# Performance work log

Hardware: AMD Instinct MI355X
Metric: run time of the kernel (lower is better)

## Reference

```python
import jax, jax.numpy as jnp
import numpy as np

B, Wd, C, H, F = 48, 88, 256, 32, 1024
NH_SELF, NH_CROSS = 8, 8


def _ln(x, g, b, eps=1e-5):
    mu = x.mean(-1, keepdims=True)
    var = ((x - mu) ** 2).mean(-1, keepdims=True)
    return (x - mu) / jnp.sqrt(var + eps) * g + b


def setup_inputs() -> dict:
    key = jax.random.key(0)
    ks = jax.random.split(key, 16)
    s = 0.02  # weight init scale
    d = {
        'pooled_features': jax.random.normal(ks[0], (B, Wd, C), jnp.float32),
        'features': jax.random.normal(ks[1], (B, C, H, Wd), jnp.float32),
        'self_pe': jax.random.normal(ks[2], (Wd, C), jnp.float32),
        'cross_pe': jax.random.normal(ks[3], (H, C), jnp.float32),
    }
    # LayerNorm params
    for n in ['ln_qs', 'ln_vs', 'ln_qc', 'ln_kv', 'ln_vc', 'ln_ffn']:
        d[n + '_g'] = jnp.ones((C,), jnp.float32)
        d[n + '_b'] = jnp.zeros((C,), jnp.float32)
    # attention projections (stored [in,out]; y = x @ W + b)
    names = ['Wq_s', 'Wk_s', 'Wv_s', 'Wp_s', 'Wq_c', 'Wk_c', 'Wv_c', 'Wp_c']
    for i, n in enumerate(names):
        d[n] = jax.random.normal(ks[4 + i], (C, C), jnp.float32) * s
    for n in ['bq_s', 'bv_s', 'bp_s', 'bq_c', 'bv_c', 'bp_c']:
        d[n] = jnp.zeros((C,), jnp.float32)
    # FFN
    d['W1'] = jax.random.normal(ks[12], (C, F), jnp.float32) * s
    d['b1'] = jnp.zeros((F,), jnp.float32)
    d['W2'] = jax.random.normal(ks[13], (F, C), jnp.float32) * s
    d['b2'] = jnp.zeros((C,), jnp.float32)
    return d


def reference(pooled_features, features, self_pe, cross_pe,
              ln_qs_g, ln_qs_b, ln_vs_g, ln_vs_b,
              ln_qc_g, ln_qc_b, ln_kv_g, ln_kv_b, ln_vc_g, ln_vc_b,
              ln_ffn_g, ln_ffn_b,
              Wq_s, bq_s, Wk_s, Wv_s, bv_s, Wp_s, bp_s,
              Wq_c, bq_c, Wk_c, Wv_c, bv_c, Wp_c, bp_c,
              W1, b1, W2, b2):
    b, w, c = pooled_features.shape
    h = features.shape[2]
    ds = c // NH_SELF
    dc = c // NH_CROSS

    # ---- cross attention first (op_order='cross_first', with_pe=True) ----
    xq = pooled_features                                  # [B,W,C]
    qn = _ln(xq, ln_qc_g, ln_qc_b)
    kv = jnp.transpose(features, (0, 3, 2, 1))            # [B,W,H,C]
    kn = _ln(kv + cross_pe[None, None], ln_kv_g, ln_kv_b)
    vn = _ln(kv, ln_vc_g, ln_vc_b)
    q = (qn @ Wq_c + bq_c).reshape(b, w, NH_CROSS, dc)    # query len 1 per column
    k = (kn @ Wk_c).reshape(b, w, h, NH_CROSS, dc)
    v = (vn @ Wv_c + bv_c).reshape(b, w, h, NH_CROSS, dc)
    attn = jnp.einsum('bwhd,bwkhd->bwhk', q, k) * (dc ** -0.5)
    attn = jax.nn.softmax(attn, axis=-1)
    out = jnp.einsum('bwhk,bwkhd->bwhd', attn, v).reshape(b, w, c)
    x = out @ Wp_c + bp_c + xq

    # ---- self attention over width tokens ----
    qn = _ln(x + self_pe[None], ln_qs_g, ln_qs_b)
    vn = _ln(x, ln_vs_g, ln_vs_b)
    q = (qn @ Wq_s + bq_s).reshape(b, w, NH_SELF, ds)
    k = (qn @ Wk_s).reshape(b, w, NH_SELF, ds)
    v = (vn @ Wv_s + bv_s).reshape(b, w, NH_SELF, ds)
    attn = jnp.einsum('bnhd,bmhd->bhnm', q, k) * (ds ** -0.5)
    attn = jax.nn.softmax(attn, axis=-1)
    out = jnp.einsum('bhnm,bmhd->bnhd', attn, v).reshape(b, w, c)
    x = out @ Wp_s + bp_s + x

    # ---- FFN (mmcv FFN, num_fcs=2, GELU, identity residual) ----
    hdn = _ln(x, ln_ffn_g, ln_ffn_b)
    hdn = jax.nn.gelu(hdn @ W1 + b1, approximate=False) @ W2 + b2
    return x + hdn
```

## Files before the change

kernel.cpp:

```cpp
#include <hip/hip_runtime.h>
#include <math.h>

#define B_   48
#define W_   88
#define C_   256
#define H_   32
#define F_   1024
#define BW_  (B_ * W_)
#define BWH_ (B_ * W_ * H_)
#define HW_  (H_ * W_)

typedef float  f32x4  __attribute__((ext_vector_type(4)));
typedef __bf16 bf16x8 __attribute__((ext_vector_type(8)));

__device__ __forceinline__ unsigned short f2bf(float f) {
  union { float f; unsigned int u; } v; v.f = f;
  unsigned int r = v.u + 0x7FFFu + ((v.u >> 16) & 1u);
  return (unsigned short)(r >> 16);
}
__device__ __forceinline__ float bf2f(unsigned short h) {
  union { unsigned int u; float f; } v; v.u = ((unsigned int)h) << 16;
  return v.f;
}
__device__ __forceinline__ unsigned int pack2(float a, float b) {
  return (unsigned int)f2bf(a) | ((unsigned int)f2bf(b) << 16);
}

__global__ __launch_bounds__(256) void wt_all(
    const float* __restrict__ Wq_s, const float* __restrict__ Wk_s,
    const float* __restrict__ Wv_s, const float* __restrict__ Wp_s,
    const float* __restrict__ W1, const float* __restrict__ W2,
    const float* __restrict__ bq_s,
    unsigned short* __restrict__ wqks, unsigned short* __restrict__ wvs,
    unsigned short* __restrict__ wps, unsigned short* __restrict__ w1t,
    unsigned short* __restrict__ w2t, float* __restrict__ bqks) {
  int blk = blockIdx.x, t = threadIdx.x;
  if (blk < 256) {
    int idx = blk * 256 + t; int o = idx >> 8, i = idx & 255;
    wqks[idx] = f2bf(Wq_s[i * 256 + o]);
  } else if (blk < 512) {
    int idx = (blk - 256) * 256 + t; int o = idx >> 8, i = idx & 255;
    wqks[65536 + idx] = f2bf(Wk_s[i * 256 + o]);
  } else if (blk < 768) {
    int idx = (blk - 512) * 256 + t; int o = idx >> 8, i = idx & 255;
    wvs[idx] = f2bf(Wv_s[i * 256 + o]);
  } else if (blk < 1024) {
    int idx = (blk - 768) * 256 + t; int o = idx >> 8, i = idx & 255;
    wps[idx] = f2bf(Wp_s[i * 256 + o]);
  } else if (blk < 2048) {
    int idx = (blk - 1024) * 256 + t; int o = idx >> 8, i = idx & 255;
    w1t[idx] = f2bf(W1[i * 1024 + o]);
  } else if (blk < 3072) {
    int idx = (blk - 2048) * 256 + t; int o = idx >> 10, i = idx & 1023;
    w2t[idx] = f2bf(W2[i * 256 + o]);
  } else {
    bqks[t] = bq_s[t];
    bqks[256 + t] = 0.f;
  }
}

__global__ __launch_bounds__(256) void mqk_build2(
    const float* __restrict__ Wq, const float* __restrict__ Wk,
    const float* __restrict__ bq,
    unsigned short* __restrict__ Mqk, float* __restrict__ bqk) {
  int h  = blockIdx.x >> 3;
  int cb = blockIdx.x & 7;
  __shared__ float wq_s[256][33];
  int t = threadIdx.x;
  int r0 = t >> 3, d4 = (t & 7) * 4;
#pragma unroll
  for (int j = 0; j < 8; j++) {
    int dp = r0 + j * 32;
    float4 v = *(const float4*)(Wq + (size_t)dp * 256 + 32 * h + d4);
    wq_s[dp][d4 + 0] = v.x; wq_s[dp][d4 + 1] = v.y;
    wq_s[dp][d4 + 2] = v.z; wq_s[dp][d4 + 3] = v.w;
  }
  int c_l = t >> 3, ln = t & 7;
  float wk[32];
  const float* wkr = Wk + (size_t)(32 * cb + c_l) * 256 + 32 * h;
#pragma unroll
  for (int j = 0; j < 8; j++) {
    float4 v = *(const float4*)(wkr + j * 4);
    wk[j * 4 + 0] = v.x; wk[j * 4 + 1] = v.y; wk[j * 4 + 2] = v.z; wk[j * 4 + 3] = v.w;
  }
  __syncthreads();
  const float scale = 0.17677669529663689f;
  int n = 256 * h + 32 * cb + c_l;
  for (int i = 0; i < 32; i++) {
    int dp = 8 * i + ln;
    float acc = 0.f;
#pragma unroll
    for (int dd = 0; dd < 32; dd++) acc += wq_s[dp][dd] * wk[dd];
    Mqk[(size_t)n * 256 + dp] = f2bf(acc * scale);
  }
  if (ln == 0) {
    float bb = 0.f;
#pragma unroll
    for (int dd = 0; dd < 32; dd++) bb += bq[32 * h + dd] * wk[dd];
    bqk[n] = bb * scale;
  }
}

__global__ __launch_bounds__(256) void mvp_build2(
    const float* __restrict__ Wv, const float* __restrict__ Wp,
    unsigned short* __restrict__ Mvp) {
  int h  = blockIdx.x >> 3;
  int db = blockIdx.x & 7;
  __shared__ float wv_s[256][33];
  int t = threadIdx.x;
  int r0 = t >> 3, d4 = (t & 7) * 4;
#pragma unroll
  for (int j = 0; j < 8; j++) {
    int c = r0 + j * 32;
    float4 v = *(const float4*)(Wv + (size_t)c * 256 + 32 * h + d4);
    wv_s[c][d4 + 0] = v.x; wv_s[c][d4 + 1] = v.y;
    wv_s[c][d4 + 2] = v.z; wv_s[c][d4 + 3] = v.w;
  }
  int d_l = t >> 3, ln = t & 7;
  int d = 32 * db + d_l;
  float wp[32];
#pragma unroll
  for (int dd = 0; dd < 32; dd++) wp[dd] = Wp[(size_t)(32 * h + dd) * 256 + d];
  __syncthreads();
  for (int i = 0; i < 32; i++) {
    int c = 8 * i + ln;
    float acc = 0.f;
#pragma unroll
    for (int dd = 0; dd < 32; dd++) acc += wv_s[c][dd] * wp[dd];
    Mvp[(size_t)d * 2048 + 256 * h + c] = f2bf(acc);
  }
}

__global__ void bvp_build(const float* __restrict__ bv, const float* __restrict__ Wp,
                          const float* __restrict__ bp, float* __restrict__ bvp) {
  int d = threadIdx.x;
  float acc = bp[d];
  for (int dp = 0; dp < 256; dp++) acc += bv[dp] * Wp[dp * 256 + d];
  bvp[d] = acc;
}

__global__ __launch_bounds__(256) void ln_transpose3(
    const float* __restrict__ features, const float* __restrict__ cross_pe,
    const float* __restrict__ g_kv, const float* __restrict__ b_kv,
    const float* __restrict__ g_vc, const float* __restrict__ b_vc,
    unsigned short* __restrict__ kn, unsigned short* __restrict__ vn) {
  int b   = blockIdx.x / 88;
  int tl  = blockIdx.x % 88;
  int hw0 = tl * 32;
  __shared__ float tileT[256][33];
  int tid = threadIdx.x;
  {
    int l4 = (tid & 7) * 4;
    int cc = tid >> 3;
    const float* fb = features + (size_t)b * C_ * HW_ + hw0;
#pragma unroll
    for (int p = 0; p < 8; p++) {
      int c = cc + p * 32;
      float4 v = *(const float4*)(fb + (size_t)c * HW_ + l4);
      tileT[c][l4 + 0] = v.x; tileT[c][l4 + 1] = v.y;
      tileT[c][l4 + 2] = v.z; tileT[c][l4 + 3] = v.w;
    }
  }
  __syncthreads();
  int row = tid >> 3, ln = tid & 7;
  int hw = hw0 + row;
  int hh = hw / 88, ww = hw - hh * 88;
  const float* per = cross_pe + hh * 256;
  float vreg[32], preg[32];
  float s1 = 0, s2 = 0, p1 = 0, p2 = 0;
#pragma unroll
  for (int k = 0; k < 4; k++) {
    int c0 = k * 64 + ln * 8;
    float4 pa = *(const float4*)(per + c0);
    float4 pb = *(const float4*)(per + c0 + 4);
    float pv[8] = {pa.x, pa.y, pa.z, pa.w, pb.x, pb.y, pb.z, pb.w};
#pragma unroll
    for (int i = 0; i < 8; i++) {
      float v  = tileT[c0 + i][row];
      float vp = v + pv[i];
      vreg[k * 8 + i] = v; preg[k * 8 + i] = pv[i];
      s1 += v;  s2 += v * v;
      p1 += vp; p2 += vp * vp;
    }
  }
#pragma unroll
  for (int m = 1; m < 8; m <<= 1) {
    s1 += __shfl_xor(s1, m, 8); s2 += __shfl_xor(s2, m, 8);
    p1 += __shfl_xor(p1, m, 8); p2 += __shfl_xor(p2, m, 8);
  }
  float mu  = s1 * (1.f / 256.f);
  float rs  = rsqrtf(s2 * (1.f / 256.f) - mu * mu + 1e-5f);
  float muk = p1 * (1.f / 256.f);
  float rsk = rsqrtf(p2 * (1.f / 256.f) - muk * muk + 1e-5f);
  size_t ro = ((size_t)b * 88 + ww) * 32 + hh;
#pragma unroll
  for (int k = 0; k < 4; k++) {
    int c0 = k * 64 + ln * 8;
    float gv[8], bv8[8], gk8[8], bk8[8];
    *(float4*)&gv[0]  = *(const float4*)(g_vc + c0); *(float4*)&gv[4]  = *(const float4*)(g_vc + c0 + 4);
    *(float4*)&bv8[0] = *(const float4*)(b_vc + c0); *(float4*)&bv8[4] = *(const float4*)(b_vc + c0 + 4);
    *(float4*)&gk8[0] = *(const float4*)(g_kv + c0); *(float4*)&gk8[4] = *(const float4*)(g_kv + c0 + 4);
    *(float4*)&bk8[0] = *(const float4*)(b_kv + c0); *(float4*)&bk8[4] = *(const float4*)(b_kv + c0 + 4);
    uint4 uv, uk;
    unsigned int pv_[4], pk_[4];
#pragma unroll
    for (int i = 0; i < 8; i += 2) {
      float cg0 = gv[i] * rs, cg1 = gv[i + 1] * rs;
      float o0 = fmaf(vreg[k * 8 + i],     cg0, fmaf(-mu, cg0, bv8[i]));
      float o1 = fmaf(vreg[k * 8 + i + 1], cg1, fmaf(-mu, cg1, bv8[i + 1]));
      pv_[i >> 1] = pack2(o0, o1);
      float ck0 = gk8[i] * rsk, ck1 = gk8[i + 1] * rsk;
      float q0 = fmaf(vreg[k * 8 + i],     ck0, fmaf(preg[k * 8 + i] - muk,     ck0, bk8[i]));
      float q1 = fmaf(vreg[k * 8 + i + 1], ck1, fmaf(preg[k * 8 + i + 1] - muk, ck1, bk8[i + 1]));
      pk_[i >> 1] = pack2(q0, q1);
    }
    uv.x = pv_[0]; uv.y = pv_[1]; uv.z = pv_[2]; uv.w = pv_[3];
    uk.x = pk_[0]; uk.y = pk_[1]; uk.z = pk_[2]; uk.w = pk_[3];
    *(uint4*)(vn + ro * 256 + c0) = uv;
    *(uint4*)(kn + ro * 256 + c0) = uk;
  }
}

__global__ __launch_bounds__(256) void ln_rows(
    const float* __restrict__ x,
    const float* __restrict__ g, const float* __restrict__ bta,
    unsigned short* __restrict__ out) {
  int row = blockIdx.x, c = threadIdx.x;
  float v = x[(size_t)row * C_ + c];
  float s1 = v, s2 = v * v;
#pragma unroll
  for (int m = 32; m > 0; m >>= 1) {
    s1 += __shfl_xor(s1, m, 64);
    s2 += __shfl_xor(s2, m, 64);
  }
  __shared__ float red[8];
  int wave = c >> 6;
  if ((c & 63) == 0) { red[wave] = s1; red[4 + wave] = s2; }
  __syncthreads();
  s1 = red[0] + red[1] + red[2] + red[3];
  s2 = red[4] + red[5] + red[6] + red[7];
  float mu = s1 * (1.f / C_);
  float rs = rsqrtf(s2 * (1.f / C_) - mu * mu + 1e-5f);
  out[(size_t)row * C_ + c] = f2bf((v - mu) * rs * g[c] + bta[c]);
}

__global__ __launch_bounds__(256) void ln_dual(
    const float* __restrict__ x, const float* __restrict__ pe,
    const float* __restrict__ g1, const float* __restrict__ b1a,
    const float* __restrict__ g2, const float* __restrict__ b2a,
    unsigned short* __restrict__ out1, unsigned short* __restrict__ out2) {
  int row = blockIdx.x, c = threadIdx.x;
  float v = x[(size_t)row * C_ + c];
  float vp = v + pe[(size_t)(row % 88) * C_ + c];
  float s1 = v, s2 = v * v, t1 = vp, t2 = vp * vp;
#pragma unroll
  for (int m = 32; m > 0; m >>= 1) {
    s1 += __shfl_xor(s1, m, 64); s2 += __shfl_xor(s2, m, 64);
    t1 += __shfl_xor(t1, m, 64); t2 += __shfl_xor(t2, m, 64);
  }
  __shared__ float red[16];
  int wave = c >> 6;
  if ((c & 63) == 0) {
    red[wave] = s1; red[4 + wave] = s2; red[8 + wave] = t1; red[12 + wave] = t2;
  }
  __syncthreads();
  s1 = red[0] + red[1] + red[2] + red[3];
  s2 = red[4] + red[5] + red[6] + red[7];
  t1 = red[8] + red[9] + red[10] + red[11];
  t2 = red[12] + red[13] + red[14] + red[15];
  float mu = s1 * (1.f / C_), rs = rsqrtf(s2 * (1.f / C_) - mu * mu + 1e-5f);
  float mup = t1 * (1.f / C_), rsp = rsqrtf(t2 * (1.f / C_) - mup * mup + 1e-5f);
  out1[(size_t)row * C_ + c] = f2bf((vp - mup) * rsp * g1[c] + b1a[c]);
  out2[(size_t)row * C_ + c] = f2bf((v - mu) * rs * g2[c] + b2a[c]);
}

__global__ __launch_bounds__(256) void gemm_bt(
    const unsigned short* __restrict__ A, const unsigned short* __restrict__ Bt,
    int M, int N, int K,
    const float* __restrict__ bias, const float* __restrict__ resid,
    float* __restrict__ outF, unsigned short* __restrict__ outB, int act_gelu) {
  __shared__ __attribute__((aligned(16))) unsigned short As[64][32];
  __shared__ __attribute__((aligned(16))) unsigned short Bs[64][32];
  const int tiles_n = N >> 6;
  const int bm = blockIdx.x / tiles_n;
  const int bn = blockIdx.x % tiles_n;
  const int tid = threadIdx.x;
  const int wave = tid >> 6, lane = tid & 63;
  const int quad = lane >> 4, lr = lane & 15;
  const int wm = (wave >> 1) << 5, wn = (wave & 1) << 5;
  const int lrow = tid >> 2;
  const int lcol = (tid & 3) << 3;
  const size_t a_base = (size_t)(bm * 64 + lrow) * K + lcol;
  const size_t b_base = (size_t)(bn * 64 + lrow) * K + lcol;
  f32x4 acc[2][2] = {};
  for (int k0 = 0; k0 < K; k0 += 32) {
    *(uint4*)&As[lrow][lcol] = *(const uint4*)(A + a_base + k0);
    *(uint4*)&Bs[lrow][lcol] = *(const uint4*)(Bt + b_base + k0);
    __syncthreads();
    bf16x8 af0 = *(const bf16x8*)&As[wm + lr][quad << 3];
    bf16x8 af1 = *(const bf16x8*)&As[wm + 16 + lr][quad << 3];
    bf16x8 bf0 = *(const bf16x8*)&Bs[wn + lr][quad << 3];
    bf16x8 bf1 = *(const bf16x8*)&Bs[wn + 16 + lr][quad << 3];
    acc[0][0] = __builtin_amdgcn_mfma_f32_16x16x32_bf16(af0, bf0, acc[0][0], 0, 0, 0);
    acc[0][1] = __builtin_amdgcn_mfma_f32_16x16x32_bf16(af0, bf1, acc[0][1], 0, 0, 0);
    acc[1][0] = __builtin_amdgcn_mfma_f32_16x16x32_bf16(af1, bf0, acc[1][0], 0, 0, 0);
    acc[1][1] = __builtin_amdgcn_mfma_f32_16x16x32_bf16(af1, bf1, acc[1][1], 0, 0, 0);
    __syncthreads();
  }
#pragma unroll
  for (int i = 0; i < 2; i++)
#pragma unroll
    for (int j = 0; j < 2; j++)
#pragma unroll
      for (int rr = 0; rr < 4; rr++) {
        int row = bm * 64 + wm + i * 16 + quad * 4 + rr;
        int col = bn * 64 + wn + j * 16 + lr;
        float val = acc[i][j][rr];
        if (bias) val += bias[col];
        if (act_gelu) val = 0.5f * val * (1.f + erff(val * 0.70710678118654752f));
        if (resid) val += resid[(size_t)row * N + col];
        if (outF) outF[(size_t)row * N + col] = val;
        else outB[(size_t)row * N + col] = f2bf(val);
      }
}

#define KSTR 264
__global__ __launch_bounds__(256) void cross_attn2(
    const unsigned short* __restrict__ qt_g,
    const unsigned short* __restrict__ kn, const unsigned short* __restrict__ vn,
    unsigned short* __restrict__ ctx_g) {
  int bw = blockIdx.x;
  int tid = threadIdx.x;
  __shared__ __attribute__((aligned(16))) unsigned short qtl[8][KSTR];
  __shared__ __attribute__((aligned(16))) unsigned short knl[32][KSTR];
  __shared__ __attribute__((aligned(16))) unsigned short vnl[32][KSTR];
  __shared__ float s_sc[32 * 9];
  __shared__ float ps[8 * 36];
  __shared__ __attribute__((aligned(16))) unsigned short ctxl[2048];
  {
    uint4 qv = *(const uint4*)(qt_g + (size_t)bw * 2048 + tid * 8);
    int h = tid >> 5, c0 = (tid & 31) * 8;
    *(uint4*)&qtl[h][c0] = qv;
    int j = tid >> 3, cs = (tid & 7) * 32;
    const unsigned short* kr = kn + ((size_t)bw * 32 + j) * 256 + cs;
    const unsigned short* vr = vn + ((size_t)bw * 32 + j) * 256 + cs;
#pragma unroll
    for (int k = 0; k < 4; k++) {
      *(uint4*)&knl[j][cs + k * 8] = *(const uint4*)(kr + k * 8);
      *(uint4*)&vnl[j][cs + k * 8] = *(const uint4*)(vr + k * 8);
    }
  }
  __syncthreads();
  {
    int j = tid >> 3, h = tid & 7;
    float acc = 0.f;
#pragma unroll
    for (int c8 = 0; c8 < 32; c8++) {
      bf16x8 kk = *(const bf16x8*)&knl[j][c8 * 8];
      bf16x8 qq = *(const bf16x8*)&qtl[h][c8 * 8];
#pragma unroll
      for (int i = 0; i < 8; i++) acc += (float)qq[i] * (float)kk[i];
    }
    s_sc[j * 9 + h] = acc;
  }
  __syncthreads();
  {
    int h = tid >> 5, j = tid & 31;
    float s = s_sc[j * 9 + h];
    float mx = s;
#pragma unroll
    for (int m = 16; m > 0; m >>= 1) mx = fmaxf(mx, __shfl_xor(mx, m, 32));
    float e = __expf(s - mx);
    float sum = e;
#pragma unroll
    for (int m = 16; m > 0; m >>= 1) sum += __shfl_xor(sum, m, 32);
    ps[h * 36 + j] = e / sum;
  }
  __syncthreads();
  {
    int h = tid & 7, c0 = (tid >> 3) * 8;
    float acc[8];
#pragma unroll
    for (int i = 0; i < 8; i++) acc[i] = 0.f;
#pragma unroll 8
    for (int j = 0; j < 32; j++) {
      float p = ps[h * 36 + j];
      bf16x8 vv = *(const bf16x8*)&vnl[j][c0];
#pragma unroll
      for (int i = 0; i < 8; i++) acc[i] += p * (float)vv[i];
    }
    unsigned short pk[8];
#pragma unroll
    for (int i = 0; i < 8; i++) pk[i] = f2bf(acc[i]);
    *(uint4*)&ctxl[h * 256 + c0] = *(uint4*)pk;
  }
  __syncthreads();
  *(uint4*)(ctx_g + (size_t)bw * 2048 + tid * 8) = *(const uint4*)&ctxl[tid * 8];
}

__global__ __launch_bounds__(64) void self_attn2(
    const float* __restrict__ qk, const float* __restrict__ v,
    unsigned short* __restrict__ out) {
  int blk = blockIdx.x;
  int half = blk & 1, h = (blk >> 1) & 7, b = blk >> 4;
  __shared__ float kl[88][32];
  __shared__ float vl[88][32];
  __shared__ float sc[44][89];
  int t = threadIdx.x;
  for (int i = t; i < 704; i += 64) {
    int m = i >> 3, d4 = (i & 7) << 2;
    *(float4*)&kl[m][d4] = *(const float4*)(qk + ((size_t)(b * 88 + m)) * 512 + 256 + h * 32 + d4);
    *(float4*)&vl[m][d4] = *(const float4*)(v + ((size_t)(b * 88 + m)) * 256 + h * 32 + d4);
  }
  __syncthreads();
  if (t < 44) {
    int r = half * 44 + t;
    const float* qrow = qk + ((size_t)(b * 88 + r)) * 512 + h * 32;
    float qr[32];
#pragma unroll
    for (int d = 0; d < 32; d++) qr[d] = qrow[d];
    float mx = -1e30f;
    for (int m = 0; m < 88; m++) {
      float s = 0.f;
#pragma unroll
      for (int d = 0; d < 32; d++) s += qr[d] * kl[m][d];
      s *= 0.17677669529663689f;
      sc[t][m] = s;
      mx = fmaxf(mx, s);
    }
    float sum = 0.f;
    for (int m = 0; m < 88; m++) { float e = __expf(sc[t][m] - mx); sc[t][m] = e; sum += e; }
    float inv = 1.f / sum;
    float o[32];
#pragma unroll
    for (int d = 0; d < 32; d++) o[d] = 0.f;
    for (int m = 0; m < 88; m++) {
      float p = sc[t][m] * inv;
#pragma unroll
      for (int d = 0; d < 32; d++) o[d] += p * vl[m][d];
    }
    unsigned short* orow = out + ((size_t)(b * 88 + r)) * 256 + h * 32;
#pragma unroll
    for (int g = 0; g < 4; g++) {
      uint4 u;
      u.x = pack2(o[g * 8 + 0], o[g * 8 + 1]);
      u.y = pack2(o[g * 8 + 2], o[g * 8 + 3]);
      u.z = pack2(o[g * 8 + 4], o[g * 8 + 5]);
      u.w = pack2(o[g * 8 + 6], o[g * 8 + 7]);
      *(uint4*)(orow + g * 8) = u;
    }
  }
}

extern "C" void kernel_launch(void* const* d_in, const int* in_sizes, int n_in,
                              void* d_out, int out_size, void* d_ws, size_t ws_size,
                              hipStream_t stream) {
  (void)in_sizes; (void)n_in; (void)out_size; (void)ws_size;
  const float* pooled   = (const float*)d_in[0];
  const float* features = (const float*)d_in[1];
  const float* self_pe  = (const float*)d_in[2];
  const float* cross_pe = (const float*)d_in[3];
  const float* ln_qs_g = (const float*)d_in[4],  *ln_qs_b = (const float*)d_in[5];
  const float* ln_vs_g = (const float*)d_in[6],  *ln_vs_b = (const float*)d_in[7];
  const float* ln_qc_g = (const float*)d_in[8],  *ln_qc_b = (const float*)d_in[9];
  const float* ln_kv_g = (const float*)d_in[10], *ln_kv_b = (const float*)d_in[11];
  const float* ln_vc_g = (const float*)d_in[12], *ln_vc_b = (const float*)d_in[13];
  const float* ln_ffn_g = (const float*)d_in[14], *ln_ffn_b = (const float*)d_in[15];
  const float* Wq_s = (const float*)d_in[16], *Wk_s = (const float*)d_in[17];
  const float* Wv_s = (const float*)d_in[18], *Wp_s = (const float*)d_in[19];
  const float* Wq_c = (const float*)d_in[20], *Wk_c = (const float*)d_in[21];
  const float* Wv_c = (const float*)d_in[22], *Wp_c = (const float*)d_in[23];
  const float* bq_s = (const float*)d_in[24], *bv_s = (const float*)d_in[25];
  const float* bp_s = (const float*)d_in[26], *bq_c = (const float*)d_in[27];
  const float* bv_c = (const float*)d_in[28], *bp_c = (const float*)d_in[29];
  const float* W1 = (const float*)d_in[30], *b1 = (const float*)d_in[31];
  const float* W2 = (const float*)d_in[32], *b2 = (const float*)d_in[33];
  float* outp = (float*)d_out;
  char* ws = (char*)d_ws;

  size_t off = 0;
  auto alloc = [&](size_t bytes) { size_t o = off; off = (off + bytes + 255) & ~(size_t)255; return o; };
  const size_t big = (size_t)BWH_ * C_ * 2;
  size_t KN  = alloc(big);
  size_t VN  = alloc(big);
  size_t QT  = alloc((size_t)BW_ * 2048 * 2);
  size_t CTX = alloc((size_t)BW_ * 2048 * 2);
  size_t MQK = alloc((size_t)2048 * 256 * 2);
  size_t MVP = alloc((size_t)256 * 2048 * 2);
  size_t BQK = alloc(2048 * 4);
  size_t BVP = alloc(256 * 4);
  size_t WQKS = alloc((size_t)512 * 256 * 2);
  size_t BQKS = alloc(512 * 4);
  size_t WVS = alloc(65536 * 2), WPS = alloc(65536 * 2);
  size_t W1T = alloc(262144 * 2), W2T = alloc(262144 * 2);
  size_t QN_C = alloc((size_t)BW_ * C_ * 2);
  size_t offp = KN;
  auto allocP = [&](size_t bytes) { size_t o = offp; offp = (offp + bytes + 255) & ~(size_t)255; return o; };
  size_t X1   = allocP((size_t)BW_ * C_ * 4);
  size_t QN_S = allocP((size_t)BW_ * C_ * 2);
  size_t VN_S = allocP((size_t)BW_ * C_ * 2);
  size_t QK_S = allocP((size_t)BW_ * 512 * 4);
  size_t V_S  = allocP((size_t)BW_ * C_ * 4);
  size_t S_O  = allocP((size_t)BW_ * C_ * 2);
  size_t X2   = allocP((size_t)BW_ * C_ * 4);
  size_t FFN  = allocP((size_t)BW_ * C_ * 2);
  size_t H1   = allocP((size_t)BW_ * F_ * 2);

  unsigned short* kn   = (unsigned short*)(ws + KN);
  unsigned short* vn   = (unsigned short*)(ws + VN);
  unsigned short* qt   = (unsigned short*)(ws + QT);
  unsigned short* ctx  = (unsigned short*)(ws + CTX);
  unsigned short* mqk  = (unsigned short*)(ws + MQK);
  unsigned short* mvp  = (unsigned short*)(ws + MVP);
  float* bqk = (float*)(ws + BQK);
  float* bvp = (float*)(ws + BVP);
  unsigned short* wqks = (unsigned short*)(ws + WQKS);
  float* bqks = (float*)(ws + BQKS);
  unsigned short* wvs = (unsigned short*)(ws + WVS), *wps = (unsigned short*)(ws + WPS);
  unsigned short* w1t = (unsigned short*)(ws + W1T), *w2t = (unsigned short*)(ws + W2T);
  unsigned short* qn_c = (unsigned short*)(ws + QN_C);
  float*          x1   = (float*)(ws + X1);
  unsigned short* qn_s = (unsigned short*)(ws + QN_S);
  unsigned short* vn_s = (unsigned short*)(ws + VN_S);
  float* qk_s = (float*)(ws + QK_S);
  float* v_s  = (float*)(ws + V_S);
  unsigned short* s_o  = (unsigned short*)(ws + S_O);
  float*          x2   = (float*)(ws + X2);
  unsigned short* ffn_n = (unsigned short*)(ws + FFN);
  unsigned short* h1    = (unsigned short*)(ws + H1);

  wt_all<<<3073, 256, 0, stream>>>(Wq_s, Wk_s, Wv_s, Wp_s, W1, W2, bq_s,
                                   wqks, wvs, wps, w1t, w2t, bqks);
  mqk_build2<<<64, 256, 0, stream>>>(Wq_c, Wk_c, bq_c, mqk, bqk);
  mvp_build2<<<64, 256, 0, stream>>>(Wv_c, Wp_c, mvp);
  bvp_build<<<1, 256, 0, stream>>>(bv_c, Wp_c, bp_c, bvp);

  ln_transpose3<<<B_ * 88, 256, 0, stream>>>(features, cross_pe,
      ln_kv_g, ln_kv_b, ln_vc_g, ln_vc_b, kn, vn);

  ln_rows<<<BW_, 256, 0, stream>>>(pooled, ln_qc_g, ln_qc_b, qn_c);
  gemm_bt<<<(BW_ / 64) * (2048 / 64), 256, 0, stream>>>(qn_c, mqk, BW_, 2048, 256,
      bqk, nullptr, nullptr, qt, 0);

  cross_attn2<<<BW_, 256, 0, stream>>>(qt, kn, vn, ctx);

  gemm_bt<<<(BW_ / 64) * (C_ / 64), 256, 0, stream>>>(ctx, mvp, BW_, C_, 2048,
      bvp, pooled, x1, nullptr, 0);

  ln_dual<<<BW_, 256, 0, stream>>>(x1, self_pe, ln_qs_g, ln_qs_b,
                                   ln_vs_g, ln_vs_b, qn_s, vn_s);

  gemm_bt<<<(BW_ / 64) * (512 / 64), 256, 0, stream>>>(qn_s, wqks, BW_, 512, 256,
      bqks, nullptr, qk_s, nullptr, 0);
  gemm_bt<<<(BW_ / 64) * (C_ / 64), 256, 0, stream>>>(vn_s, wvs, BW_, C_, 256,
      bv_s, nullptr, v_s, nullptr, 0);

  self_attn2<<<B_ * 16, 64, 0, stream>>>(qk_s, v_s, s_o);

  gemm_bt<<<(BW_ / 64) * (C_ / 64), 256, 0, stream>>>(s_o, wps, BW_, C_, C_,
      bp_s, x1, x2, nullptr, 0);

  ln_rows<<<BW_, 256, 0, stream>>>(x2, ln_ffn_g, ln_ffn_b, ffn_n);
  gemm_bt<<<(BW_ / 64) * (F_ / 64), 256, 0, stream>>>(ffn_n, w1t, BW_, F_, C_,
      b1, nullptr, nullptr, h1, 1);
  gemm_bt<<<(BW_ / 64) * (C_ / 64), 256, 0, stream>>>(h1, w2t, BW_, C_, F_,
      b2, x2, outp, nullptr, 0);
}
```

Measured before the change: 562.6 us.

## Merge weight-prep and query LayerNorm kernels, prefetch GEMM tiles, rework self-attention

```diff
diff --git a/kernel.cpp b/kernel.cpp
--- a/kernel.cpp
+++ b/kernel.cpp
@@ -26,198 +26,205 @@
   return (unsigned int)f2bf(a) | ((unsigned int)f2bf(b) << 16);
 }
 
-__global__ __launch_bounds__(256) void wt_all(
+__global__ __launch_bounds__(256) void prep_all(
     const float* __restrict__ Wq_s, const float* __restrict__ Wk_s,
     const float* __restrict__ Wv_s, const float* __restrict__ Wp_s,
     const float* __restrict__ W1, const float* __restrict__ W2,
-    const float* __restrict__ bq_s,
-    unsigned short* __restrict__ wqks, unsigned short* __restrict__ wvs,
-    unsigned short* __restrict__ wps, unsigned short* __restrict__ w1t,
-    unsigned short* __restrict__ w2t, float* __restrict__ bqks) {
+    const float* __restrict__ Wq_c, const float* __restrict__ Wk_c,
+    const float* __restrict__ Wv_c, const float* __restrict__ Wp_c,
+    const float* __restrict__ bq_s, const float* __restrict__ bv_s,
+    const float* __restrict__ bq_c, const float* __restrict__ bv_c,
+    const float* __restrict__ bp_c,
+    const float* __restrict__ pooled,
+    const float* __restrict__ ln_qc_g, const float* __restrict__ ln_qc_b,
+    unsigned short* __restrict__ wqkvs, unsigned short* __restrict__ wps,
+    unsigned short* __restrict__ w1t, unsigned short* __restrict__ w2t,
+    unsigned short* __restrict__ mqk, unsigned short* __restrict__ mvp,
+    float* __restrict__ bqk, float* __restrict__ bvp,
+    float* __restrict__ bqkvs, unsigned short* __restrict__ qn_c) {
+  __shared__ float smem[256 * 33 + 4 * 33];
   int blk = blockIdx.x, t = threadIdx.x;
-  if (blk < 256) {
-    int idx = blk * 256 + t; int o = idx >> 8, i = idx & 255;
-    wqks[idx] = f2bf(Wq_s[i * 256 + o]);
-  } else if (blk < 512) {
-    int idx = (blk - 256) * 256 + t; int o = idx >> 8, i = idx & 255;
-    wqks[65536 + idx] = f2bf(Wk_s[i * 256 + o]);
-  } else if (blk < 768) {
-    int idx = (blk - 512) * 256 + t; int o = idx >> 8, i = idx & 255;
-    wvs[idx] = f2bf(Wv_s[i * 256 + o]);
-  } else if (blk < 1024) {
-    int idx = (blk - 768) * 256 + t; int o = idx >> 8, i = idx & 255;
-    wps[idx] = f2bf(Wp_s[i * 256 + o]);
-  } else if (blk < 2048) {
-    int idx = (blk - 1024) * 256 + t; int o = idx >> 8, i = idx & 255;
-    w1t[idx] = f2bf(W1[i * 1024 + o]);
-  } else if (blk < 3072) {
-    int idx = (blk - 2048) * 256 + t; int o = idx >> 10, i = idx & 1023;
-    w2t[idx] = f2bf(W2[i * 256 + o]);
+
+  if (blk < 768) {
+    const float* src; unsigned short* dst; int Cc, R, tile;
+    if (blk < 64)       { src = Wq_s; dst = wqkvs;          Cc = 256;  R = 256;  tile = blk; }
+    else if (blk < 128) { src = Wk_s; dst = wqkvs + 65536;  Cc = 256;  R = 256;  tile = blk - 64; }
+    else if (blk < 192) { src = Wv_s; dst = wqkvs + 131072; Cc = 256;  R = 256;  tile = blk - 128; }
+    else if (blk < 256) { src = Wp_s; dst = wps;            Cc = 256;  R = 256;  tile = blk - 192; }
+    else if (blk < 512) { src = W1;   dst = w1t;            Cc = 1024; R = 256;  tile = blk - 256; }
+    else                { src = W2;   dst = w2t;            Cc = 256;  R = 1024; tile = blk - 512; }
+    int tcn = Cc >> 5;
+    int tr = tile / tcn, tc = tile % tcn;
+    float (*lds)[33] = (float(*)[33])smem;
+    int r = t >> 3, c4 = (t & 7) * 4;
+    float4 v = *(const float4*)(src + (size_t)(tr * 32 + r) * Cc + tc * 32 + c4);
+    lds[r][c4 + 0] = v.x; lds[r][c4 + 1] = v.y; lds[r][c4 + 2] = v.z; lds[r][c4 + 3] = v.w;
+    __syncthreads();
+    int rd = t >> 3, cd4 = (t & 7) * 4;
+    unsigned int u0 = pack2(lds[cd4 + 0][rd], lds[cd4 + 1][rd]);
+    unsigned int u1 = pack2(lds[cd4 + 2][rd], lds[cd4 + 3][rd]);
+    uint2 u; u.x = u0; u.y = u1;
+    *(uint2*)(dst + (size_t)(tc * 32 + rd) * R + tr * 32 + cd4) = u;
+  } else if (blk < 1280) {
+    int lb = blk - 768;
+    int h = lb >> 6, cb = lb & 63;
+    float (*wq)[33] = (float(*)[33])smem;
+    float (*wk)[33] = (float(*)[33])(smem + 256 * 33);
+#pragma unroll
+    for (int p = 0; p < 8; p++) {
+      int dp = (t >> 3) + 32 * p, d4 = (t & 7) * 4;
+      float4 v = *(const float4*)(Wq_c + (size_t)dp * 256 + 32 * h + d4);
+      wq[dp][d4 + 0] = v.x; wq[dp][d4 + 1] = v.y; wq[dp][d4 + 2] = v.z; wq[dp][d4 + 3] = v.w;
+    }
+    if (t < 128) {
+      int c_l = t >> 5, dd = t & 31;
+      wk[c_l][dd] = Wk_c[(size_t)(cb * 4 + c_l) * 256 + 32 * h + dd];
+    }
+    __syncthreads();
+    const float scale = 0.17677669529663689f;
+    int c_l = t >> 6, ln = t & 63;
+    int n = 256 * h + cb * 4 + c_l;
+#pragma unroll
+    for (int j = 0; j < 4; j++) {
+      int dp = ln + 64 * j;
+      float acc = 0.f;
+#pragma unroll
+      for (int dd = 0; dd < 32; dd++) acc += wq[dp][dd] * wk[c_l][dd];
+      mqk[(size_t)n * 256 + dp] = f2bf(acc * scale);
+    }
+    if (ln == 0) {
+      float bb = 0.f;
+#pragma unroll
+      for (int dd = 0; dd < 32; dd++) bb += bq_c[32 * h + dd] * wk[c_l][dd];
+      bqk[n] = bb * scale;
+    }
+  } else if (blk < 1792) {
+    int lb = blk - 1280;
+    int h = lb >> 6, db = lb & 63;
+    float (*wv)[33] = (float(*)[33])smem;
+    float (*wp)[33] = (float(*)[33])(smem + 256 * 33);
+#pragma unroll
+    for (int p = 0; p < 8; p++) {
+      int c = (t >> 3) + 32 * p, d4 = (t & 7) * 4;
+      float4 v = *(const float4*)(Wv_c + (size_t)c * 256 + 32 * h + d4);
+      wv[c][d4 + 0] = v.x; wv[c][d4 + 1] = v.y; wv[c][d4 + 2] = v.z; wv[c][d4 + 3] = v.w;
+    }
+    if (t < 128) {
+      int d_l = t >> 5, dd = t & 31;
+      wp[d_l][dd] = Wp_c[(size_t)(32 * h + dd) * 256 + db * 4 + d_l];
+    }
+    __syncthreads();
+    int d_l = t >> 6, ln = t & 63;
+    int d = db * 4 + d_l;
+#pragma unroll
+    for (int j = 0; j < 4; j++) {
+      int c = ln + 64 * j;
+      float acc = 0.f;
+#pragma unroll
+      for (int dd = 0; dd < 32; dd++) acc += wv[c][dd] * wp[d_l][dd];
+      mvp[(size_t)d * 2048 + 256 * h + c] = f2bf(acc);
+    }
+  } else if (blk == 1792) {
+    float acc = bp_c[t];
+    for (int dp = 0; dp < 256; dp++) acc += bv_c[dp] * Wp_c[(size_t)dp * 256 + t];
+    bvp[t] = acc;
+    bqkvs[t] = bq_s[t]; bqkvs[256 + t] = 0.f; bqkvs[512 + t] = bv_s[t];
   } else {
-    bqks[t] = bq_s[t];
-    bqks[256 + t] = 0.f;
-  }
-}
-
-__global__ __launch_bounds__(256) void mqk_build2(
-    const float* __restrict__ Wq, const float* __restrict__ Wk,
-    const float* __restrict__ bq,
-    unsigned short* __restrict__ Mqk, float* __restrict__ bqk) {
-  int h  = blockIdx.x >> 3;
-  int cb = blockIdx.x & 7;
-  __shared__ float wq_s[256][33];
-  int t = threadIdx.x;
-  int r0 = t >> 3, d4 = (t & 7) * 4;
-#pragma unroll
-  for (int j = 0; j < 8; j++) {
-    int dp = r0 + j * 32;
-    float4 v = *(const float4*)(Wq + (size_t)dp * 256 + 32 * h + d4);
-    wq_s[dp][d4 + 0] = v.x; wq_s[dp][d4 + 1] = v.y;
-    wq_s[dp][d4 + 2] = v.z; wq_s[dp][d4 + 3] = v.w;
-  }
-  int c_l = t >> 3, ln = t & 7;
-  float wk[32];
-  const float* wkr = Wk + (size_t)(32 * cb + c_l) * 256 + 32 * h;
-#pragma unroll
-  for (int j = 0; j < 8; j++) {
-    float4 v = *(const float4*)(wkr + j * 4);
-    wk[j * 4 + 0] = v.x; wk[j * 4 + 1] = v.y; wk[j * 4 + 2] = v.z; wk[j * 4 + 3] = v.w;
-  }
-  __syncthreads();
-  const float scale = 0.17677669529663689f;
-  int n = 256 * h + 32 * cb + c_l;
-  for (int i = 0; i < 32; i++) {
-    int dp = 8 * i + ln;
-    float acc = 0.f;
-#pragma unroll
-    for (int dd = 0; dd < 32; dd++) acc += wq_s[dp][dd] * wk[dd];
-    Mqk[(size_t)n * 256 + dp] = f2bf(acc * scale);
-  }
-  if (ln == 0) {
-    float bb = 0.f;
-#pragma unroll
-    for (int dd = 0; dd < 32; dd++) bb += bq[32 * h + dd] * wk[dd];
-    bqk[n] = bb * scale;
-  }
-}
-
-__global__ __launch_bounds__(256) void mvp_build2(
-    const float* __restrict__ Wv, const float* __restrict__ Wp,
-    unsigned short* __restrict__ Mvp) {
-  int h  = blockIdx.x >> 3;
-  int db = blockIdx.x & 7;
-  __shared__ float wv_s[256][33];
-  int t = threadIdx.x;
-  int r0 = t >> 3, d4 = (t & 7) * 4;
-#pragma unroll
-  for (int j = 0; j < 8; j++) {
-    int c = r0 + j * 32;
-    float4 v = *(const float4*)(Wv + (size_t)c * 256 + 32 * h + d4);
-    wv_s[c][d4 + 0] = v.x; wv_s[c][d4 + 1] = v.y;
-    wv_s[c][d4 + 2] = v.z; wv_s[c][d4 + 3] = v.w;
-  }
-  int d_l = t >> 3, ln = t & 7;
-  int d = 32 * db + d_l;
-  float wp[32];
-#pragma unroll
-  for (int dd = 0; dd < 32; dd++) wp[dd] = Wp[(size_t)(32 * h + dd) * 256 + d];
-  __syncthreads();
-  for (int i = 0; i < 32; i++) {
-    int c = 8 * i + ln;
-    float acc = 0.f;
-#pragma unroll
-    for (int dd = 0; dd < 32; dd++) acc += wv_s[c][dd] * wp[dd];
-    Mvp[(size_t)d * 2048 + 256 * h + c] = f2bf(acc);
-  }
-}
-
-__global__ void bvp_build(const float* __restrict__ bv, const float* __restrict__ Wp,
-                          const float* __restrict__ bp, float* __restrict__ bvp) {
-  int d = threadIdx.x;
-  float acc = bp[d];
-  for (int dp = 0; dp < 256; dp++) acc += bv[dp] * Wp[dp * 256 + d];
-  bvp[d] = acc;
-}
-
-__global__ __launch_bounds__(256) void ln_transpose3(
+    int row = blk - 1793, c = t;
+    float v = pooled[(size_t)row * C_ + c];
+    float s1 = v, s2 = v * v;
+#pragma unroll
+    for (int m = 32; m > 0; m >>= 1) {
+      s1 += __shfl_xor(s1, m, 64); s2 += __shfl_xor(s2, m, 64);
+    }
+    float* red = smem;
+    int wave = c >> 6;
+    if ((c & 63) == 0) { red[wave] = s1; red[4 + wave] = s2; }
+    __syncthreads();
+    s1 = red[0] + red[1] + red[2] + red[3];
+    s2 = red[4] + red[5] + red[6] + red[7];
+    float mu = s1 * (1.f / C_);
+    float rs = rsqrtf(s2 * (1.f / C_) - mu * mu + 1e-5f);
+    qn_c[(size_t)row * C_ + c] = f2bf((v - mu) * rs * ln_qc_g[c] + ln_qc_b[c]);
+  }
+}
+
+__global__ __launch_bounds__(256) void ln_transpose4(
     const float* __restrict__ features, const float* __restrict__ cross_pe,
     const float* __restrict__ g_kv, const float* __restrict__ b_kv,
     const float* __restrict__ g_vc, const float* __restrict__ b_vc,
     unsigned short* __restrict__ kn, unsigned short* __restrict__ vn) {
-  int b   = blockIdx.x / 88;
-  int tl  = blockIdx.x % 88;
-  int hw0 = tl * 32;
-  __shared__ float tileT[256][33];
-  int tid = threadIdx.x;
+  int b   = blockIdx.x / 176;
+  int tl  = blockIdx.x % 176;
+  int hw0 = tl * 16;
+  __shared__ float tileT[256][17];
+  int t = threadIdx.x;
   {
-    int l4 = (tid & 7) * 4;
-    int cc = tid >> 3;
+    int a  = (t & 3) * 4;
+    int cc = t >> 2;
     const float* fb = features + (size_t)b * C_ * HW_ + hw0;
 #pragma unroll
-    for (int p = 0; p < 8; p++) {
-      int c = cc + p * 32;
-      float4 v = *(const float4*)(fb + (size_t)c * HW_ + l4);
-      tileT[c][l4 + 0] = v.x; tileT[c][l4 + 1] = v.y;
-      tileT[c][l4 + 2] = v.z; tileT[c][l4 + 3] = v.w;
-    }
-  }
-  __syncthreads();
-  int row = tid >> 3, ln = tid & 7;
+    for (int p = 0; p < 4; p++) {
+      int c = cc + p * 64;
+      float4 v = *(const float4*)(fb + (size_t)c * HW_ + a);
+      tileT[c][a + 0] = v.x; tileT[c][a + 1] = v.y;
+      tileT[c][a + 2] = v.z; tileT[c][a + 3] = v.w;
+    }
+  }
+  __syncthreads();
+  int row = t >> 4, ln = t & 15;
   int hw = hw0 + row;
   int hh = hw / 88, ww = hw - hh * 88;
   const float* per = cross_pe + hh * 256;
-  float vreg[32], preg[32];
+  float vreg[16], preg[16];
   float s1 = 0, s2 = 0, p1 = 0, p2 = 0;
 #pragma unroll
-  for (int k = 0; k < 4; k++) {
-    int c0 = k * 64 + ln * 8;
-    float4 pa = *(const float4*)(per + c0);
-    float4 pb = *(const float4*)(per + c0 + 4);
-    float pv[8] = {pa.x, pa.y, pa.z, pa.w, pb.x, pb.y, pb.z, pb.w};
-#pragma unroll
-    for (int i = 0; i < 8; i++) {
+  for (int j = 0; j < 4; j++) {
+    int c0 = 4 * ln + 64 * j;
+    float4 pv = *(const float4*)(per + c0);
+    float pa[4] = {pv.x, pv.y, pv.z, pv.w};
+#pragma unroll
+    for (int i = 0; i < 4; i++) {
       float v  = tileT[c0 + i][row];
-      float vp = v + pv[i];
-      vreg[k * 8 + i] = v; preg[k * 8 + i] = pv[i];
+      float vp = v + pa[i];
+      vreg[4 * j + i] = v; preg[4 * j + i] = pa[i];
       s1 += v;  s2 += v * v;
       p1 += vp; p2 += vp * vp;
     }
   }
 #pragma unroll
-  for (int m = 1; m < 8; m <<= 1) {
-    s1 += __shfl_xor(s1, m, 8); s2 += __shfl_xor(s2, m, 8);
-    p1 += __shfl_xor(p1, m, 8); p2 += __shfl_xor(p2, m, 8);
+  for (int m = 1; m < 16; m <<= 1) {
+    s1 += __shfl_xor(s1, m, 16); s2 += __shfl_xor(s2, m, 16);
+    p1 += __shfl_xor(p1, m, 16); p2 += __shfl_xor(p2, m, 16);
   }
   float mu  = s1 * (1.f / 256.f);
   float rs  = rsqrtf(s2 * (1.f / 256.f) - mu * mu + 1e-5f);
   float muk = p1 * (1.f / 256.f);
   float rsk = rsqrtf(p2 * (1.f / 256.f) - muk * muk + 1e-5f);
   size_t ro = ((size_t)b * 88 + ww) * 32 + hh;
-#pragma unroll
-  for (int k = 0; k < 4; k++) {
-    int c0 = k * 64 + ln * 8;
-    float gv[8], bv8[8], gk8[8], bk8[8];
-    *(float4*)&gv[0]  = *(const float4*)(g_vc + c0); *(float4*)&gv[4]  = *(const float4*)(g_vc + c0 + 4);
-    *(float4*)&bv8[0] = *(const float4*)(b_vc + c0); *(float4*)&bv8[4] = *(const float4*)(b_vc + c0 + 4);
-    *(float4*)&gk8[0] = *(const float4*)(g_kv + c0); *(float4*)&gk8[4] = *(const float4*)(g_kv + c0 + 4);
-    *(float4*)&bk8[0] = *(const float4*)(b_kv + c0); *(float4*)&bk8[4] = *(const float4*)(b_kv + c0 + 4);
-    uint4 uv, uk;
-    unsigned int pv_[4], pk_[4];
-#pragma unroll
-    for (int i = 0; i < 8; i += 2) {
-      float cg0 = gv[i] * rs, cg1 = gv[i + 1] * rs;
-      float o0 = fmaf(vreg[k * 8 + i],     cg0, fmaf(-mu, cg0, bv8[i]));
-      float o1 = fmaf(vreg[k * 8 + i + 1], cg1, fmaf(-mu, cg1, bv8[i + 1]));
-      pv_[i >> 1] = pack2(o0, o1);
-      float ck0 = gk8[i] * rsk, ck1 = gk8[i + 1] * rsk;
-      float q0 = fmaf(vreg[k * 8 + i],     ck0, fmaf(preg[k * 8 + i] - muk,     ck0, bk8[i]));
-      float q1 = fmaf(vreg[k * 8 + i + 1], ck1, fmaf(preg[k * 8 + i + 1] - muk, ck1, bk8[i + 1]));
-      pk_[i >> 1] = pack2(q0, q1);
-    }
-    uv.x = pv_[0]; uv.y = pv_[1]; uv.z = pv_[2]; uv.w = pv_[3];
-    uk.x = pk_[0]; uk.y = pk_[1]; uk.z = pk_[2]; uk.w = pk_[3];
-    *(uint4*)(vn + ro * 256 + c0) = uv;
-    *(uint4*)(kn + ro * 256 + c0) = uk;
+  unsigned short* vrow = vn + ro * 256;
+  unsigned short* krow = kn + ro * 256;
+#pragma unroll
+  for (int j = 0; j < 4; j++) {
+    int c0 = 4 * ln + 64 * j;
+    float4 gv = *(const float4*)(g_vc + c0);
+    float4 bv = *(const float4*)(b_vc + c0);
+    float4 gk = *(const float4*)(g_kv + c0);
+    float4 bk = *(const float4*)(b_kv + c0);
+    float gva[4] = {gv.x, gv.y, gv.z, gv.w}, bva[4] = {bv.x, bv.y, bv.z, bv.w};
+    float gka[4] = {gk.x, gk.y, gk.z, gk.w}, bka[4] = {bk.x, bk.y, bk.z, bk.w};
+    float ov[4], ok[4];
+#pragma unroll
+    for (int i = 0; i < 4; i++) {
+      float v = vreg[4 * j + i], p = preg[4 * j + i];
+      ov[i] = (v - mu) * rs * gva[i] + bva[i];
+      ok[i] = (v + p - muk) * rsk * gka[i] + bka[i];
+    }
+    uint2 uv, uk;
+    uv.x = pack2(ov[0], ov[1]); uv.y = pack2(ov[2], ov[3]);
+    uk.x = pack2(ok[0], ok[1]); uk.y = pack2(ok[2], ok[3]);
+    *(uint2*)(vrow + c0) = uv;
+    *(uint2*)(krow + c0) = uk;
   }
 }
 
@@ -293,10 +300,16 @@
   const size_t a_base = (size_t)(bm * 64 + lrow) * K + lcol;
   const size_t b_base = (size_t)(bn * 64 + lrow) * K + lcol;
   f32x4 acc[2][2] = {};
+  uint4 areg = *(const uint4*)(A + a_base);
+  uint4 breg = *(const uint4*)(Bt + b_base);
   for (int k0 = 0; k0 < K; k0 += 32) {
-    *(uint4*)&As[lrow][lcol] = *(const uint4*)(A + a_base + k0);
-    *(uint4*)&Bs[lrow][lcol] = *(const uint4*)(Bt + b_base + k0);
-    __syncthreads();
+    *(uint4*)&As[lrow][lcol] = areg;
+    *(uint4*)&Bs[lrow][lcol] = breg;
+    __syncthreads();
+    if (k0 + 32 < K) {
+      areg = *(const uint4*)(A + a_base + k0 + 32);
+      breg = *(const uint4*)(Bt + b_base + k0 + 32);
+    }
     bf16x8 af0 = *(const bf16x8*)&As[wm + lr][quad << 3];
     bf16x8 af1 = *(const bf16x8*)&As[wm + 16 + lr][quad << 3];
     bf16x8 bf0 = *(const bf16x8*)&Bs[wn + lr][quad << 3];
@@ -321,6 +334,56 @@
         if (resid) val += resid[(size_t)row * N + col];
         if (outF) outF[(size_t)row * N + col] = val;
         else outB[(size_t)row * N + col] = f2bf(val);
+      }
+}
+
+__global__ __launch_bounds__(256) void gemm_bt_st(
+    const unsigned short* __restrict__ A, const unsigned short* __restrict__ Bt,
+    int M, int N, int K, int ldc,
+    const float* __restrict__ bias, float* __restrict__ outF) {
+  __shared__ __attribute__((aligned(16))) unsigned short As[64][32];
+  __shared__ __attribute__((aligned(16))) unsigned short Bs[64][32];
+  const int tiles_n = N >> 6;
+  const int bm = blockIdx.x / tiles_n;
+  const int bn = blockIdx.x % tiles_n;
+  const int tid = threadIdx.x;
+  const int wave = tid >> 6, lane = tid & 63;
+  const int quad = lane >> 4, lr = lane & 15;
+  const int wm = (wave >> 1) << 5, wn = (wave & 1) << 5;
+  const int lrow = tid >> 2;
+  const int lcol = (tid & 3) << 3;
+  const size_t a_base = (size_t)(bm * 64 + lrow) * K + lcol;
+  const size_t b_base = (size_t)(bn * 64 + lrow) * K + lcol;
+  f32x4 acc[2][2] = {};
+  uint4 areg = *(const uint4*)(A + a_base);
+  uint4 breg = *(const uint4*)(Bt + b_base);
+  for (int k0 = 0; k0 < K; k0 += 32) {
+    *(uint4*)&As[lrow][lcol] = areg;
+    *(uint4*)&Bs[lrow][lcol] = breg;
+    __syncthreads();
+    if (k0 + 32 < K) {
+      areg = *(const uint4*)(A + a_base + k0 + 32);
+      breg = *(const uint4*)(Bt + b_base + k0 + 32);
+    }
+    bf16x8 af0 = *(const bf16x8*)&As[wm + lr][quad << 3];
+    bf16x8 af1 = *(const bf16x8*)&As[wm + 16 + lr][quad << 3];
+    bf16x8 bf0 = *(const bf16x8*)&Bs[wn + lr][quad << 3];
+    bf16x8 bf1 = *(const bf16x8*)&Bs[wn + 16 + lr][quad << 3];
+    acc[0][0] = __builtin_amdgcn_mfma_f32_16x16x32_bf16(af0, bf0, acc[0][0], 0, 0, 0);
+    acc[0][1] = __builtin_amdgcn_mfma_f32_16x16x32_bf16(af0, bf1, acc[0][1], 0, 0, 0);
+    acc[1][0] = __builtin_amdgcn_mfma_f32_16x16x32_bf16(af1, bf0, acc[1][0], 0, 0, 0);
+    acc[1][1] = __builtin_amdgcn_mfma_f32_16x16x32_bf16(af1, bf1, acc[1][1], 0, 0, 0);
+    __syncthreads();
+  }
+#pragma unroll
+  for (int i = 0; i < 2; i++)
+#pragma unroll
+    for (int j = 0; j < 2; j++)
+#pragma unroll
+      for (int rr = 0; rr < 4; rr++) {
+        int row = bm * 64 + wm + i * 16 + quad * 4 + rr;
+        int col = bn * 64 + wn + j * 16 + lr;
+        outF[(size_t)row * ldc + col] = acc[i][j][rr] + bias[col];
       }
 }
 
@@ -398,57 +461,67 @@
   *(uint4*)(ctx_g + (size_t)bw * 2048 + tid * 8) = *(const uint4*)&ctxl[tid * 8];
 }
 
-__global__ __launch_bounds__(64) void self_attn2(
-    const float* __restrict__ qk, const float* __restrict__ v,
-    unsigned short* __restrict__ out) {
-  int blk = blockIdx.x;
-  int half = blk & 1, h = (blk >> 1) & 7, b = blk >> 4;
-  __shared__ float kl[88][32];
-  __shared__ float vl[88][32];
-  __shared__ float sc[44][89];
+__global__ __launch_bounds__(192) void self_attn3(
+    const float* __restrict__ qkv, unsigned short* __restrict__ out) {
+  int b = blockIdx.x >> 3;
+  int h = blockIdx.x & 7;
   int t = threadIdx.x;
-  for (int i = t; i < 704; i += 64) {
+  __shared__ float kl[88][33];
+  __shared__ float vl[88][33];
+  for (int i = t; i < 704; i += 192) {
     int m = i >> 3, d4 = (i & 7) << 2;
-    *(float4*)&kl[m][d4] = *(const float4*)(qk + ((size_t)(b * 88 + m)) * 512 + 256 + h * 32 + d4);
-    *(float4*)&vl[m][d4] = *(const float4*)(v + ((size_t)(b * 88 + m)) * 256 + h * 32 + d4);
-  }
-  __syncthreads();
-  if (t < 44) {
-    int r = half * 44 + t;
-    const float* qrow = qk + ((size_t)(b * 88 + r)) * 512 + h * 32;
+    float4 kv4 = *(const float4*)(qkv + (size_t)(b * 88 + m) * 768 + 256 + h * 32 + d4);
+    float4 vv4 = *(const float4*)(qkv + (size_t)(b * 88 + m) * 768 + 512 + h * 32 + d4);
+    kl[m][d4 + 0] = kv4.x; kl[m][d4 + 1] = kv4.y; kl[m][d4 + 2] = kv4.z; kl[m][d4 + 3] = kv4.w;
+    vl[m][d4 + 0] = vv4.x; vl[m][d4 + 1] = vv4.y; vl[m][d4 + 2] = vv4.z; vl[m][d4 + 3] = vv4.w;
+  }
+  __syncthreads();
+  int r = t >> 1, dh = t & 1;
+  if (r < 88) {
+    const float* qrow = qkv + (size_t)(b * 88 + r) * 768 + h * 32;
     float qr[32];
 #pragma unroll
-    for (int d = 0; d < 32; d++) qr[d] = qrow[d];
+    for (int g = 0; g < 8; g++) {
+      float4 q4 = *(const float4*)(qrow + g * 4);
+      qr[g * 4 + 0] = q4.x; qr[g * 4 + 1] = q4.y; qr[g * 4 + 2] = q4.z; qr[g * 4 + 3] = q4.w;
+    }
+    float sreg[44];
     float mx = -1e30f;
-    for (int m = 0; m < 88; m++) {
+    int m0 = dh * 44;
+    for (int mi = 0; mi < 44; mi++) {
+      const float* krow = kl[m0 + mi];
       float s = 0.f;
 #pragma unroll
-      for (int d = 0; d < 32; d++) s += qr[d] * kl[m][d];
+      for (int d = 0; d < 32; d++) s += qr[d] * krow[d];
       s *= 0.17677669529663689f;
-      sc[t][m] = s;
+      sreg[mi] = s;
       mx = fmaxf(mx, s);
     }
+    mx = fmaxf(mx, __shfl_xor(mx, 1, 64));
     float sum = 0.f;
-    for (int m = 0; m < 88; m++) { float e = __expf(sc[t][m] - mx); sc[t][m] = e; sum += e; }
+    for (int mi = 0; mi < 44; mi++) { float e = __expf(sreg[mi] - mx); sreg[mi] = e; sum += e; }
+    sum += __shfl_xor(sum, 1, 64);
     float inv = 1.f / sum;
     float o[32];
 #pragma unroll
     for (int d = 0; d < 32; d++) o[d] = 0.f;
-    for (int m = 0; m < 88; m++) {
-      float p = sc[t][m] * inv;
-#pragma unroll
-      for (int d = 0; d < 32; d++) o[d] += p * vl[m][d];
-    }
-    unsigned short* orow = out + ((size_t)(b * 88 + r)) * 256 + h * 32;
-#pragma unroll
-    for (int g = 0; g < 4; g++) {
-      uint4 u;
-      u.x = pack2(o[g * 8 + 0], o[g * 8 + 1]);
-      u.y = pack2(o[g * 8 + 2], o[g * 8 + 3]);
-      u.z = pack2(o[g * 8 + 4], o[g * 8 + 5]);
-      u.w = pack2(o[g * 8 + 6], o[g * 8 + 7]);
-      *(uint4*)(orow + g * 8) = u;
-    }
+    for (int mi = 0; mi < 44; mi++) {
+      float p = sreg[mi] * inv;
+      const float* vrow = vl[m0 + mi];
+#pragma unroll
+      for (int d = 0; d < 32; d++) o[d] += p * vrow[d];
+    }
+#pragma unroll
+    for (int d = 0; d < 32; d++) o[d] += __shfl_xor(o[d], 1, 64);
+    unsigned short* orow = out + (size_t)(b * 88 + r) * 256 + h * 32 + dh * 16;
+    uint4 u0, u1;
+    int d0 = dh * 16;
+    u0.x = pack2(o[d0 + 0], o[d0 + 1]);  u0.y = pack2(o[d0 + 2], o[d0 + 3]);
+    u0.z = pack2(o[d0 + 4], o[d0 + 5]);  u0.w = pack2(o[d0 + 6], o[d0 + 7]);
+    u1.x = pack2(o[d0 + 8], o[d0 + 9]);  u1.y = pack2(o[d0 + 10], o[d0 + 11]);
+    u1.z = pack2(o[d0 + 12], o[d0 + 13]); u1.w = pack2(o[d0 + 14], o[d0 + 15]);
+    *(uint4*)(orow) = u0;
+    *(uint4*)(orow + 8) = u1;
   }
 }
 
@@ -489,22 +562,21 @@
   size_t MVP = alloc((size_t)256 * 2048 * 2);
   size_t BQK = alloc(2048 * 4);
   size_t BVP = alloc(256 * 4);
-  size_t WQKS = alloc((size_t)512 * 256 * 2);
-  size_t BQKS = alloc(512 * 4);
-  size_t WVS = alloc(65536 * 2), WPS = alloc(65536 * 2);
+  size_t WQKVS = alloc((size_t)768 * 256 * 2);
+  size_t BQKVS = alloc(768 * 4);
+  size_t WPS = alloc(65536 * 2);
   size_t W1T = alloc(262144 * 2), W2T = alloc(262144 * 2);
   size_t QN_C = alloc((size_t)BW_ * C_ * 2);
   size_t offp = KN;
   auto allocP = [&](size_t bytes) { size_t o = offp; offp = (offp + bytes + 255) & ~(size_t)255; return o; };
-  size_t X1   = allocP((size_t)BW_ * C_ * 4);
-  size_t QN_S = allocP((size_t)BW_ * C_ * 2);
-  size_t VN_S = allocP((size_t)BW_ * C_ * 2);
-  size_t QK_S = allocP((size_t)BW_ * 512 * 4);
-  size_t V_S  = allocP((size_t)BW_ * C_ * 4);
-  size_t S_O  = allocP((size_t)BW_ * C_ * 2);
-  size_t X2   = allocP((size_t)BW_ * C_ * 4);
-  size_t FFN  = allocP((size_t)BW_ * C_ * 2);
-  size_t H1   = allocP((size_t)BW_ * F_ * 2);
+  size_t X1    = allocP((size_t)BW_ * C_ * 4);
+  size_t QN_S  = allocP((size_t)BW_ * C_ * 2);
+  size_t VN_S  = allocP((size_t)BW_ * C_ * 2);
+  size_t QKV_S = allocP((size_t)BW_ * 768 * 4);
+  size_t S_O   = allocP((size_t)BW_ * C_ * 2);
+  size_t X2    = allocP((size_t)BW_ * C_ * 4);
+  size_t FFN   = allocP((size_t)BW_ * C_ * 2);
+  size_t H1    = allocP((size_t)BW_ * F_ * 2);
 
   unsigned short* kn   = (unsigned short*)(ws + KN);
   unsigned short* vn   = (unsigned short*)(ws + VN);
@@ -514,31 +586,28 @@
   unsigned short* mvp  = (unsigned short*)(ws + MVP);
   float* bqk = (float*)(ws + BQK);
   float* bvp = (float*)(ws + BVP);
-  unsigned short* wqks = (unsigned short*)(ws + WQKS);
-  float* bqks = (float*)(ws + BQKS);
-  unsigned short* wvs = (unsigned short*)(ws + WVS), *wps = (unsigned short*)(ws + WPS);
+  unsigned short* wqkvs = (unsigned short*)(ws + WQKVS);
+  float* bqkvs = (float*)(ws + BQKVS);
+  unsigned short* wps = (unsigned short*)(ws + WPS);
   unsigned short* w1t = (unsigned short*)(ws + W1T), *w2t = (unsigned short*)(ws + W2T);
   unsigned short* qn_c = (unsigned short*)(ws + QN_C);
   float*          x1   = (float*)(ws + X1);
   unsigned short* qn_s = (unsigned short*)(ws + QN_S);
   unsigned short* vn_s = (unsigned short*)(ws + VN_S);
-  float* qk_s = (float*)(ws + QK_S);
-  float* v_s  = (float*)(ws + V_S);
+  float* qkv_s = (float*)(ws + QKV_S);
   unsigned short* s_o  = (unsigned short*)(ws + S_O);
   float*          x2   = (float*)(ws + X2);
   unsigned short* ffn_n = (unsigned short*)(ws + FFN);
   unsigned short* h1    = (unsigned short*)(ws + H1);
 
-  wt_all<<<3073, 256, 0, stream>>>(Wq_s, Wk_s, Wv_s, Wp_s, W1, W2, bq_s,
-                                   wqks, wvs, wps, w1t, w2t, bqks);
-  mqk_build2<<<64, 256, 0, stream>>>(Wq_c, Wk_c, bq_c, mqk, bqk);
-  mvp_build2<<<64, 256, 0, stream>>>(Wv_c, Wp_c, mvp);
-  bvp_build<<<1, 256, 0, stream>>>(bv_c, Wp_c, bp_c, bvp);
-
-  ln_transpose3<<<B_ * 88, 256, 0, stream>>>(features, cross_pe,
+  prep_all<<<6017, 256, 0, stream>>>(
+      Wq_s, Wk_s, Wv_s, Wp_s, W1, W2, Wq_c, Wk_c, Wv_c, Wp_c,
+      bq_s, bv_s, bq_c, bv_c, bp_c, pooled, ln_qc_g, ln_qc_b,
+      wqkvs, wps, w1t, w2t, mqk, mvp, bqk, bvp, bqkvs, qn_c);
+
+  ln_transpose4<<<B_ * 176, 256, 0, stream>>>(features, cross_pe,
       ln_kv_g, ln_kv_b, ln_vc_g, ln_vc_b, kn, vn);
 
-  ln_rows<<<BW_, 256, 0, stream>>>(pooled, ln_qc_g, ln_qc_b, qn_c);
   gemm_bt<<<(BW_ / 64) * (2048 / 64), 256, 0, stream>>>(qn_c, mqk, BW_, 2048, 256,
       bqk, nullptr, nullptr, qt, 0);
 
@@ -550,12 +619,12 @@
   ln_dual<<<BW_, 256, 0, stream>>>(x1, self_pe, ln_qs_g, ln_qs_b,
                                    ln_vs_g, ln_vs_b, qn_s, vn_s);
 
-  gemm_bt<<<(BW_ / 64) * (512 / 64), 256, 0, stream>>>(qn_s, wqks, BW_, 512, 256,
-      bqks, nullptr, qk_s, nullptr, 0);
-  gemm_bt<<<(BW_ / 64) * (C_ / 64), 256, 0, stream>>>(vn_s, wvs, BW_, C_, 256,
-      bv_s, nullptr, v_s, nullptr, 0);
-
-  self_attn2<<<B_ * 16, 64, 0, stream>>>(qk_s, v_s, s_o);
+  gemm_bt_st<<<(BW_ / 64) * (512 / 64), 256, 0, stream>>>(qn_s, wqkvs, BW_, 512, 256,
+      768, bqkvs, qkv_s);
+  gemm_bt_st<<<(BW_ / 64) * (256 / 64), 256, 0, stream>>>(vn_s, wqkvs + 131072, BW_, 256, 256,
+      768, bqkvs + 512, qkv_s + 512);
+
+  self_attn3<<<B_ * 8, 192, 0, stream>>>(qkv_s, s_o);
 
   gemm_bt<<<(BW_ / 64) * (C_ / 64), 256, 0, stream>>>(s_o, wps, BW_, C_, C_,
       bp_s, x1, x2, nullptr, 0);
```

After: 532.7 us. -5.3%, faster.
